# Kernel tuning notes

Hardware: AMD Instinct MI355X
Metric: run time of the kernel (lower is better)

## Reference

```python
import jax, jax.numpy as jnp
import numpy as np

N_USERS = 100000
N_ITEMS = 50000
N = N_USERS + N_ITEMS
EMBED_DIM = 64
N_LAYERS = 3
NNZ = 4800000


def setup_inputs() -> dict:
    key = jax.random.key(0)
    k1, k2, k3, k4, k5 = jax.random.split(key, 5)
    user_emb = jax.random.normal(k1, (N_USERS, EMBED_DIM), dtype=jnp.float32)
    item_emb = jax.random.normal(k2, (N_ITEMS, EMBED_DIM), dtype=jnp.float32)
    adj_row = jax.random.randint(k3, (NNZ,), 0, N, dtype=jnp.int32)
    adj_col = jax.random.randint(k4, (NNZ,), 0, N, dtype=jnp.int32)
    # normalized adjacency values (positive, small) like D^-1/2 A D^-1/2
    adj_vals = jax.random.uniform(k5, (NNZ,), dtype=jnp.float32) * 0.05
    return {"user_emb": user_emb, "item_emb": item_emb,
            "adj_row": adj_row, "adj_col": adj_col, "adj_vals": adj_vals}


def _spmm(vals, row, col, x):
    # sparse (N,N) @ dense (N,d) via gather + segment_sum
    return jax.ops.segment_sum(vals[:, None] * x[col], row, num_segments=N)


def reference(user_emb, item_emb, adj_row, adj_col, adj_vals):
    all_emb = jnp.concatenate([user_emb, item_emb], axis=0)  # (N, d)
    acc = all_emb  # running sum of layer outputs (fused mean)
    cur = all_emb
    for _ in range(N_LAYERS):
        cur = _spmm(adj_vals, adj_row, adj_col, cur)
        acc = acc + cur
    final_emb = acc / jnp.float32(N_LAYERS + 1)
    return final_emb[:N_USERS], final_emb[N_USERS:]
```

## Files before the change

### kernel.cpp

```cpp
#include <hip/hip_runtime.h>

#define N_USERS 100000
#define N_ITEMS 50000
#define N_TOTAL 150000
#define DIM 64
#define NNZ_C 4800000
#define NELEM (N_TOTAL * DIM)
#define NELEM4 (NELEM / 4)

#define RPB 74
#define NB 2048
#define NBLK 512
#define CHUNK (NNZ_C / NBLK)
#define CAP 4096

typedef unsigned short ush;

__device__ __forceinline__ float bf2f(ush u) {
    return __uint_as_float(((unsigned)u) << 16);
}
__device__ __forceinline__ ush f2bf(float f) {
    unsigned u = __float_as_uint(f);
    return (ush)((u + 0x7fffu + ((u >> 16) & 1u)) >> 16);
}

__global__ __launch_bounds__(256) void init_kernel(
    const float4* __restrict__ user, const float4* __restrict__ item,
    ushort4* __restrict__ A16, float4* __restrict__ out) {
    int i = blockIdx.x * 256 + threadIdx.x;
    if (i >= NELEM4) return;
    const int u4 = N_USERS * DIM / 4;
    float4 v = (i < u4) ? user[i] : item[i - u4];
    ushort4 b;
    b.x = f2bf(v.x); b.y = f2bf(v.y); b.z = f2bf(v.z); b.w = f2bf(v.w);
    A16[i] = b;
    out[i] = v;
}

__global__ __launch_bounds__(1024) void p1_hist(
    const int* __restrict__ row, int* __restrict__ histmat) {
    __shared__ int h[NB];
    int t = threadIdx.x, b = blockIdx.x;
    for (int j = t; j < NB; j += 1024) h[j] = 0;
    __syncthreads();
    int kbeg = b * CHUNK, kend = kbeg + CHUNK;
    for (int k = kbeg + t; k < kend; k += 1024) {
        unsigned r = (unsigned)row[k];
        atomicAdd(&h[r / RPB], 1);
    }
    __syncthreads();
    for (int j = t; j < NB; j += 1024) histmat[b * NB + j] = h[j];
}

__global__ __launch_bounds__(256) void p2a_colscan(
    const int* __restrict__ histmat, int* __restrict__ basemat,
    int* __restrict__ T) {
    int j = blockIdx.x * 256 + threadIdx.x;
    int run = 0;
    for (int b = 0; b < NBLK; b++) {
        basemat[b * NB + j] = run;
        run += histmat[b * NB + j];
    }
    T[j] = run;
}

__global__ __launch_bounds__(1024) void p2b_scan(
    const int* __restrict__ T, int* __restrict__ bucketbase,
    int* __restrict__ rowptr) {
    __shared__ int s[1024];
    int t = threadIdx.x;
    int v0 = T[2 * t], v1 = T[2 * t + 1];
    int pair = v0 + v1;
    s[t] = pair;
    __syncthreads();
    for (int off = 1; off < 1024; off <<= 1) {
        int w = (t >= off) ? s[t - off] : 0;
        __syncthreads();
        s[t] += w;
        __syncthreads();
    }
    int excl = s[t] - pair;
    bucketbase[2 * t] = excl;
    bucketbase[2 * t + 1] = excl + v0;
    if (t == 1023) { bucketbase[NB] = s[t]; rowptr[N_TOTAL] = NNZ_C; }
}

__global__ __launch_bounds__(1024) void p3_scatter(
    const int* __restrict__ row, const int* __restrict__ col,
    const float* __restrict__ vals, const int* __restrict__ basemat,
    const int* __restrict__ bucketbase, uint2* __restrict__ entries) {
    __shared__ int lbase[NB];
    int t = threadIdx.x, b = blockIdx.x;
    for (int j = t; j < NB; j += 1024)
        lbase[j] = bucketbase[j] + basemat[b * NB + j];
    __syncthreads();
    int kbeg = b * CHUNK, kend = kbeg + CHUNK;
    for (int k = kbeg + t; k < kend; k += 1024) {
        unsigned r = (unsigned)row[k];
        unsigned j = r / RPB;
        unsigned rl = r - j * RPB;
        int slot = atomicAdd(&lbase[j], 1);
        entries[slot] = make_uint2((rl << 18) | (unsigned)col[k],
                                   __float_as_uint(vals[k]));
    }
}

__global__ __launch_bounds__(512) void p4_sort(
    const int* __restrict__ bucketbase, uint2* __restrict__ entries,
    int* __restrict__ rowptr) {
    __shared__ uint2 stage[CAP];
    __shared__ int cnt[128], scanb[128], wp[128];
    int t = threadIdx.x, b = blockIdx.x;
    int base = bucketbase[b];
    int n = bucketbase[b + 1] - base;
    if (n > CAP) n = CAP;
    if (t < 128) cnt[t] = 0;
    __syncthreads();
    for (int i = t; i < n; i += 512) {
        uint2 e = entries[base + i];
        stage[i] = e;
        atomicAdd(&cnt[e.x >> 18], 1);
    }
    __syncthreads();
    if (t < 128) scanb[t] = cnt[t];
    __syncthreads();
    for (int off = 1; off < 128; off <<= 1) {
        int w = 0;
        if (t < 128 && t >= off) w = scanb[t - off];
        __syncthreads();
        if (t < 128) scanb[t] += w;
        __syncthreads();
    }
    if (t < RPB) {
        int excl = scanb[t] - cnt[t];
        wp[t] = excl;
        int rg = b * RPB + t;
        if (rg < N_TOTAL) rowptr[rg] = base + excl;
    }
    __syncthreads();
    for (int i = t; i < n; i += 512) {
        uint2 e = stage[i];
        unsigned rl = e.x >> 18;
        int pos = atomicAdd(&wp[rl], 1);
        ((int2*)entries)[base + pos] =
            make_int2((int)(e.x & 0x3FFFFu), (int)e.y);
    }
}

__global__ __launch_bounds__(256) void spmm_csr_kernel(
    const int* __restrict__ rowptr, const int2* __restrict__ csr,
    const ushort4* __restrict__ x4, ushort4* __restrict__ y4) {
    int gid = blockIdx.x * 256 + threadIdx.x;
    int lane = threadIdx.x & 63;
    int group = lane >> 4;
    int chunk = lane & 15;
    int r = (gid >> 6) * 4 + group;
    if (r >= N_TOTAL) return;
    int start = rowptr[r], end = rowptr[r + 1];
    float4 acc = make_float4(0.f, 0.f, 0.f, 0.f);
    for (int j0 = start; j0 < end; j0 += 16) {
        int j = j0 + chunk;
        int2 pair = make_int2(0, 0);
        if (j < end) pair = csr[j];
        int cnt = min(16, end - j0);
        #pragma unroll 4
        for (int t = 0; t < cnt; t++) {
            int src = group * 16 + t;
            int cc = __shfl(pair.x, src);
            float vv = __int_as_float(__shfl(pair.y, src));
            ushort4 xv = x4[cc * 16 + chunk];
            acc.x += vv * bf2f(xv.x);
            acc.y += vv * bf2f(xv.y);
            acc.z += vv * bf2f(xv.z);
            acc.w += vv * bf2f(xv.w);
        }
    }
    int o = r * 16 + chunk;
    ushort4 yb;
    yb.x = f2bf(acc.x); yb.y = f2bf(acc.y);
    yb.z = f2bf(acc.z); yb.w = f2bf(acc.w);
    y4[o] = yb;
}

__global__ __launch_bounds__(256) void merge_kernel(
    float4* __restrict__ out, const ushort4* __restrict__ e1,
    const ushort4* __restrict__ e2, const ushort4* __restrict__ e3) {
    int i = blockIdx.x * 256 + threadIdx.x;
    if (i >= NELEM4) return;
    float4 o = out[i];
    ushort4 a = e1[i], b = e2[i], c = e3[i];
    o.x = (o.x + bf2f(a.x) + bf2f(b.x) + bf2f(c.x)) * 0.25f;
    o.y = (o.y + bf2f(a.y) + bf2f(b.y) + bf2f(c.y)) * 0.25f;
    o.z = (o.z + bf2f(a.z) + bf2f(b.z) + bf2f(c.z)) * 0.25f;
    o.w = (o.w + bf2f(a.w) + bf2f(b.w) + bf2f(c.w)) * 0.25f;
    out[i] = o;
}

extern "C" void kernel_launch(void* const* d_in, const int* in_sizes, int n_in,
                              void* d_out, int out_size, void* d_ws, size_t ws_size,
                              hipStream_t stream) {
    const float* user_emb = (const float*)d_in[0];
    const float* item_emb = (const float*)d_in[1];
    const int*   adj_row  = (const int*)d_in[2];
    const int*   adj_col  = (const int*)d_in[3];
    const float* adj_vals = (const float*)d_in[4];
    float* out = (float*)d_out;

    ush*   A          = (ush*)d_ws;
    ush*   B          = A + NELEM;
    ush*   C          = B + NELEM;
    uint2* entries    = (uint2*)(C + NELEM);
    int*   histmat    = (int*)(entries + NNZ_C);
    int*   basemat    = histmat + NBLK * NB;
    int*   T          = basemat + NBLK * NB;
    int*   bucketbase = T + NB;
    int*   rowptr     = bucketbase + NB + 1;

    const int eltBlocks  = (NELEM4 + 255) / 256;
    const int spmmBlocks = N_TOTAL / 16;

    init_kernel<<<eltBlocks, 256, 0, stream>>>(
        (const float4*)user_emb, (const float4*)item_emb,
        (ushort4*)A, (float4*)out);
    p1_hist<<<NBLK, 1024, 0, stream>>>(adj_row, histmat);
    p2a_colscan<<<NB / 256, 256, 0, stream>>>(histmat, basemat, T);
    p2b_scan<<<1, 1024, 0, stream>>>(T, bucketbase, rowptr);
    p3_scatter<<<NBLK, 1024, 0, stream>>>(adj_row, adj_col, adj_vals,
                                          basemat, bucketbase, entries);
    p4_sort<<<NB, 512, 0, stream>>>(bucketbase, entries, rowptr);

    spmm_csr_kernel<<<spmmBlocks, 256, 0, stream>>>(rowptr, (const int2*)entries,
        (const ushort4*)A, (ushort4*)B);
    spmm_csr_kernel<<<spmmBlocks, 256, 0, stream>>>(rowptr, (const int2*)entries,
        (const ushort4*)B, (ushort4*)C);
    spmm_csr_kernel<<<spmmBlocks, 256, 0, stream>>>(rowptr, (const int2*)entries,
        (const ushort4*)C, (ushort4*)A);
    merge_kernel<<<eltBlocks, 256, 0, stream>>>(
        (float4*)out, (const ushort4*)B, (const ushort4*)C, (const ushort4*)A);
}
```

Before: 616.2 us.

## Fuse final SpMM with layer merge and locally sort scatter in shared memory

The last SpMM layer now folds the averaging into its epilogue and writes the fp32 output directly. This removes the separate merge kernel and the fp32 copy of the input embeddings that init used to write. The scatter phase now counting-sorts each block's chunk into shared memory and then writes to the global buckets in sorted order, so global writes are grouped by bucket. The merge now uses the bf16-rounded input embeddings instead of the fp32 originals, which costs a little accuracy. The large shared-memory footprint in the scatter kernel limits occupancy.

```diff
diff --git a/kernel.cpp b/kernel.cpp
--- a/kernel.cpp
+++ b/kernel.cpp
@@ -26,7 +26,7 @@
 
 __global__ __launch_bounds__(256) void init_kernel(
     const float4* __restrict__ user, const float4* __restrict__ item,
-    ushort4* __restrict__ A16, float4* __restrict__ out) {
+    ushort4* __restrict__ A16) {
     int i = blockIdx.x * 256 + threadIdx.x;
     if (i >= NELEM4) return;
     const int u4 = N_USERS * DIM / 4;
@@ -34,7 +34,6 @@
     ushort4 b;
     b.x = f2bf(v.x); b.y = f2bf(v.y); b.z = f2bf(v.z); b.w = f2bf(v.w);
     A16[i] = b;
-    out[i] = v;
 }
 
 __global__ __launch_bounds__(1024) void p1_hist(
@@ -87,22 +86,47 @@
 
 __global__ __launch_bounds__(1024) void p3_scatter(
     const int* __restrict__ row, const int* __restrict__ col,
-    const float* __restrict__ vals, const int* __restrict__ basemat,
-    const int* __restrict__ bucketbase, uint2* __restrict__ entries) {
-    __shared__ int lbase[NB];
+    const float* __restrict__ vals, const int* __restrict__ histmat,
+    const int* __restrict__ basemat, const int* __restrict__ bucketbase,
+    uint2* __restrict__ entries) {
+    __shared__ int s[1024];
+    __shared__ int wp[NB];
+    __shared__ int gbase[NB];
+    __shared__ uint2 sorted[CHUNK];
+    __shared__ int dest[CHUNK];
     int t = threadIdx.x, b = blockIdx.x;
-    for (int j = t; j < NB; j += 1024)
-        lbase[j] = bucketbase[j] + basemat[b * NB + j];
-    __syncthreads();
+
+    int c0 = histmat[b * NB + 2 * t];
+    int c1 = histmat[b * NB + 2 * t + 1];
+    int pair = c0 + c1;
+    s[t] = pair;
+    __syncthreads();
+    for (int off = 1; off < 1024; off <<= 1) {
+        int w = (t >= off) ? s[t - off] : 0;
+        __syncthreads();
+        s[t] += w;
+        __syncthreads();
+    }
+    int excl = s[t] - pair;
+    wp[2 * t] = excl;
+    wp[2 * t + 1] = excl + c0;
+    gbase[2 * t]     = bucketbase[2 * t]     + basemat[b * NB + 2 * t]     - excl;
+    gbase[2 * t + 1] = bucketbase[2 * t + 1] + basemat[b * NB + 2 * t + 1] - (excl + c0);
+    __syncthreads();
+
     int kbeg = b * CHUNK, kend = kbeg + CHUNK;
     for (int k = kbeg + t; k < kend; k += 1024) {
         unsigned r = (unsigned)row[k];
         unsigned j = r / RPB;
         unsigned rl = r - j * RPB;
-        int slot = atomicAdd(&lbase[j], 1);
-        entries[slot] = make_uint2((rl << 18) | (unsigned)col[k],
-                                   __float_as_uint(vals[k]));
-    }
+        int pos = atomicAdd(&wp[j], 1);
+        sorted[pos] = make_uint2((rl << 18) | (unsigned)col[k],
+                                 __float_as_uint(vals[k]));
+        dest[pos] = gbase[j] + pos;
+    }
+    __syncthreads();
+    for (int i = t; i < CHUNK; i += 1024)
+        entries[dest[i]] = sorted[i];
 }
 
 __global__ __launch_bounds__(512) void p4_sort(
@@ -182,18 +206,43 @@
     y4[o] = yb;
 }
 
-__global__ __launch_bounds__(256) void merge_kernel(
-    float4* __restrict__ out, const ushort4* __restrict__ e1,
-    const ushort4* __restrict__ e2, const ushort4* __restrict__ e3) {
-    int i = blockIdx.x * 256 + threadIdx.x;
-    if (i >= NELEM4) return;
-    float4 o = out[i];
-    ushort4 a = e1[i], b = e2[i], c = e3[i];
-    o.x = (o.x + bf2f(a.x) + bf2f(b.x) + bf2f(c.x)) * 0.25f;
-    o.y = (o.y + bf2f(a.y) + bf2f(b.y) + bf2f(c.y)) * 0.25f;
-    o.z = (o.z + bf2f(a.z) + bf2f(b.z) + bf2f(c.z)) * 0.25f;
-    o.w = (o.w + bf2f(a.w) + bf2f(b.w) + bf2f(c.w)) * 0.25f;
-    out[i] = o;
+__global__ __launch_bounds__(256) void spmm_merge_kernel(
+    const int* __restrict__ rowptr, const int2* __restrict__ csr,
+    const ushort4* __restrict__ x4 , const ushort4* __restrict__ e0,
+    const ushort4* __restrict__ e1, float4* __restrict__ out) {
+    int gid = blockIdx.x * 256 + threadIdx.x;
+    int lane = threadIdx.x & 63;
+    int group = lane >> 4;
+    int chunk = lane & 15;
+    int r = (gid >> 6) * 4 + group;
+    if (r >= N_TOTAL) return;
+    int start = rowptr[r], end = rowptr[r + 1];
+    float4 acc = make_float4(0.f, 0.f, 0.f, 0.f);
+    for (int j0 = start; j0 < end; j0 += 16) {
+        int j = j0 + chunk;
+        int2 pair = make_int2(0, 0);
+        if (j < end) pair = csr[j];
+        int cnt = min(16, end - j0);
+        #pragma unroll 4
+        for (int t = 0; t < cnt; t++) {
+            int src = group * 16 + t;
+            int cc = __shfl(pair.x, src);
+            float vv = __int_as_float(__shfl(pair.y, src));
+            ushort4 xv = x4[cc * 16 + chunk];
+            acc.x += vv * bf2f(xv.x);
+            acc.y += vv * bf2f(xv.y);
+            acc.z += vv * bf2f(xv.z);
+            acc.w += vv * bf2f(xv.w);
+        }
+    }
+    int o = r * 16 + chunk;
+    ushort4 a = e0[o], b = e1[o], c = x4[o];
+    float4 oo;
+    oo.x = (bf2f(a.x) + bf2f(b.x) + bf2f(c.x) + acc.x) * 0.25f;
+    oo.y = (bf2f(a.y) + bf2f(b.y) + bf2f(c.y) + acc.y) * 0.25f;
+    oo.z = (bf2f(a.z) + bf2f(b.z) + bf2f(c.z) + acc.z) * 0.25f;
+    oo.w = (bf2f(a.w) + bf2f(b.w) + bf2f(c.w) + acc.w) * 0.25f;
+    out[o] = oo;
 }
 
 extern "C" void kernel_launch(void* const* d_in, const int* in_sizes, int n_in,
@@ -220,21 +269,18 @@
     const int spmmBlocks = N_TOTAL / 16;
 
     init_kernel<<<eltBlocks, 256, 0, stream>>>(
-        (const float4*)user_emb, (const float4*)item_emb,
-        (ushort4*)A, (float4*)out);
+        (const float4*)user_emb, (const float4*)item_emb, (ushort4*)A);
     p1_hist<<<NBLK, 1024, 0, stream>>>(adj_row, histmat);
     p2a_colscan<<<NB / 256, 256, 0, stream>>>(histmat, basemat, T);
     p2b_scan<<<1, 1024, 0, stream>>>(T, bucketbase, rowptr);
     p3_scatter<<<NBLK, 1024, 0, stream>>>(adj_row, adj_col, adj_vals,
-                                          basemat, bucketbase, entries);
+                                          histmat, basemat, bucketbase, entries);
     p4_sort<<<NB, 512, 0, stream>>>(bucketbase, entries, rowptr);
 
     spmm_csr_kernel<<<spmmBlocks, 256, 0, stream>>>(rowptr, (const int2*)entries,
         (const ushort4*)A, (ushort4*)B);
     spmm_csr_kernel<<<spmmBlocks, 256, 0, stream>>>(rowptr, (const int2*)entries,
         (const ushort4*)B, (ushort4*)C);
-    spmm_csr_kernel<<<spmmBlocks, 256, 0, stream>>>(rowptr, (const int2*)entries,
-        (const ushort4*)C, (ushort4*)A);
-    merge_kernel<<<eltBlocks, 256, 0, stream>>>(
-        (float4*)out, (const ushort4*)B, (const ushort4*)C, (const ushort4*)A);
-}
+    spmm_merge_kernel<<<spmmBlocks, 256, 0, stream>>>(rowptr, (const int2*)entries,
+        (const ushort4*)C, (const ushort4*)A, (const ushort4*)B, (float4*)out);
+}
```

Measured after the change: 537.5 us. 12.8% less time.
